# Optimization experiments

Hardware: AMD Instinct MI355X
Metric: run time of the kernel (lower is better)

Reference implementation:

```python
import jax, jax.numpy as jnp
import numpy as np

N_QUBITS = 10
BATCH = 16384
Q_DEPTH = 2


def _apply_1q_shared(state, U, q):
    # state: [B, 2, 2, ..., 2]; U: [2, 2] complex, acting on wire q
    state = jnp.moveaxis(state, 1 + q, -1)
    state = jnp.einsum('b...i,ji->b...j', state, U)
    return jnp.moveaxis(state, -1, 1 + q)


def _apply_ry_batched(state, angles, q):
    # per-sample RY(angle) on wire q; angles: [B] float
    c = jnp.cos(angles * 0.5).astype(jnp.complex64)
    s = jnp.sin(angles * 0.5).astype(jnp.complex64)
    U = jnp.stack([jnp.stack([c, -s], -1), jnp.stack([s, c], -1)], -2)  # [B,2,2]
    state = jnp.moveaxis(state, 1 + q, -1)
    state = jnp.einsum('b...i,bji->b...j', state, U)
    return jnp.moveaxis(state, -1, 1 + q)


def _rot_matrix(phi, theta, omega):
    # PennyLane Rot = RZ(omega) @ RY(theta) @ RZ(phi)
    c = jnp.cos(theta * 0.5)
    s = jnp.sin(theta * 0.5)
    m00 = jnp.exp(-0.5j * (phi + omega)) * c
    m01 = -jnp.exp(0.5j * (phi - omega)) * s
    m10 = jnp.exp(-0.5j * (phi - omega)) * s
    m11 = jnp.exp(0.5j * (phi + omega)) * c
    return jnp.stack([jnp.stack([m00, m01]), jnp.stack([m10, m11])]).astype(jnp.complex64)


def _apply_cnot(state, c, t):
    st = jnp.moveaxis(state, (1 + c, 1 + t), (1, 2))  # [B, ctrl, tgt, ...]
    st = jnp.stack([st[:, 0], st[:, 1, ::-1]], axis=1)  # flip target where ctrl=1
    return jnp.moveaxis(st, (1, 2), (1 + c, 1 + t))


def setup_inputs() -> dict:
    key = jax.random.key(0)
    k1, k2 = jax.random.split(key)
    x = jax.random.uniform(k1, (BATCH, N_QUBITS), dtype=jnp.float32) * np.pi
    q_weights = 0.01 * jax.random.normal(k2, (Q_DEPTH, N_QUBITS, 3), dtype=jnp.float32)
    return {"x": x, "q_weights": q_weights}


def reference(x, q_weights) -> jnp.ndarray:
    B, n = x.shape
    L = q_weights.shape[0]
    # |0...0> statevector, batched: [B] + [2]*n (axis q <-> wire q, wire 0 most significant)
    state = jnp.zeros((B, 2 ** n), jnp.complex64).at[:, 0].set(1.0)
    state = state.reshape((B,) + (2,) * n)
    # AngleEmbedding(rotation='Y')
    for q in range(n):
        state = _apply_ry_batched(state, x[:, q], q)
    # StronglyEntanglingLayers: Rot on each wire, then ring of CNOTs with range (l % (n-1)) + 1
    for l in range(L):
        for q in range(n):
            U = _rot_matrix(q_weights[l, q, 0], q_weights[l, q, 1], q_weights[l, q, 2])
            state = _apply_1q_shared(state, U, q)
        r = (l % (n - 1)) + 1
        for q in range(n):
            state = _apply_cnot(state, q, (q + r) % n)
    probs = jnp.abs(state.reshape(B, 2 ** n)) ** 2  # [B, 2^n]
    bits = (np.arange(2 ** n)[:, None] >> (n - 1 - np.arange(n))[None, :]) & 1
    signs = jnp.asarray(1.0 - 2.0 * bits, jnp.float32)  # [2^n, n], PauliZ eigenvalues
    return (probs @ signs).astype(jnp.float32)  # [B, n] expvals
```

## Files before the change

### kernel.cpp

```cpp
#include <hip/hip_runtime.h>

#define DEVINL __device__ __forceinline__

typedef float f32x2 __attribute__((ext_vector_type(2)));

struct GC { int laneXor, regXor, rowL, rowR; };
struct Circ { GC g[20]; int sgnL[10], sgnR[10]; };

constexpr Circ build_circ() {
    Circ c{};
    unsigned A[10] = {};
    for (int i = 0; i < 10; ++i) A[i] = 1u << i;
    for (int w = 0; w < 10; ++w) {
        int pos = 9 - w;
        unsigned m = 1u << pos;
        c.g[w] = GC{ int(m >> 4), int(m & 15u), int(m >> 4), int(m & 15u) };
    }
    for (int q = 0; q < 10; ++q) { int pc = 9 - q, pt = 9 - ((q + 1) % 10); A[pt] ^= A[pc]; }
    unsigned M[10] = {}, Inv[10] = {};
    for (int i = 0; i < 10; ++i) { M[i] = A[i]; Inv[i] = 1u << i; }
    for (int col = 0; col < 10; ++col) {
        int piv = col;
        while (!((M[piv] >> col) & 1u)) ++piv;
        unsigned tm = M[col]; M[col] = M[piv]; M[piv] = tm;
        unsigned ti = Inv[col]; Inv[col] = Inv[piv]; Inv[piv] = ti;
        for (int r = 0; r < 10; ++r)
            if (r != col && ((M[r] >> col) & 1u)) { M[r] ^= M[col]; Inv[r] ^= Inv[col]; }
    }
    for (int w = 0; w < 10; ++w) {
        int pos = 9 - w;
        unsigned m = 0;
        for (int i = 0; i < 10; ++i) m |= ((Inv[i] >> pos) & 1u) << i;
        unsigned row = A[pos];
        c.g[10 + w] = GC{ int(m >> 4), int(m & 15u), int(row >> 4), int(row & 15u) };
    }
    for (int q = 0; q < 10; ++q) { int pc = 9 - q, pt = 9 - ((q + 2) % 10); A[pt] ^= A[pc]; }
    for (int q = 0; q < 10; ++q) { unsigned row = A[9 - q]; c.sgnL[q] = int(row >> 4); c.sgnR[q] = int(row & 15u); }
    return c;
}

constexpr Circ CC = build_circ();

static_assert(CC.g[10].rowL == 31 && CC.g[10].rowR == 15, "w0 row");
static_assert(CC.g[11].rowL == 48 && CC.g[11].rowR == 0,  "w1 row");
static_assert(CC.g[12].rowL == 56 && CC.g[12].rowR == 0,  "w2 row");
static_assert(CC.g[13].rowL == 60 && CC.g[13].rowR == 0,  "w3 row");
static_assert(CC.g[14].rowL == 62 && CC.g[14].rowR == 0,  "w4 row");
static_assert(CC.g[15].rowL == 63 && CC.g[15].rowR == 0,  "w5 row");
static_assert(CC.g[16].rowL == 63 && CC.g[16].rowR == 8,  "w6 row");
static_assert(CC.g[17].rowL == 63 && CC.g[17].rowR == 12, "w7 row");
static_assert(CC.g[18].rowL == 63 && CC.g[18].rowR == 14, "w8 row");
static_assert(CC.g[19].rowL == 63 && CC.g[19].rowR == 15, "w9 row");
static_assert(CC.g[10].laneXor == 48 && CC.g[10].regXor == 0, "w0 m");
static_assert(CC.g[11].laneXor == 24 && CC.g[12].laneXor == 12, "w1/w2 m");
static_assert(CC.g[13].laneXor == 6  && CC.g[14].laneXor == 3,  "w3/w4 m");
static_assert(CC.g[15].laneXor == 1  && CC.g[15].regXor == 8,   "w5 m");
static_assert(CC.g[16].laneXor == 0 && CC.g[16].regXor == 12, "w6 m");
static_assert(CC.g[17].laneXor == 0 && CC.g[17].regXor == 6,  "w7 m");
static_assert(CC.g[18].laneXor == 0 && CC.g[18].regXor == 3,  "w8 m");
static_assert(CC.g[19].laneXor == 48 && CC.g[19].regXor == 1,   "w9 m");

#if __has_builtin(__builtin_amdgcn_permlane32_swap)
#define HAS_PL32 1
#else
#define HAS_PL32 0
#endif
#if __has_builtin(__builtin_amdgcn_permlane16_swap)
#define HAS_PL16 1
#else
#define HAS_PL16 0
#endif

DEVINL float csw(float v, int sw) {
    return __int_as_float(__float_as_int(v) ^ sw);
}

DEVINL float bsum16(float v, int lane) {
#if HAS_PL16
    auto r = __builtin_amdgcn_permlane16_swap(__float_as_int(v), __float_as_int(v), false, false);
    return __int_as_float(r[0]) + __int_as_float(r[1]);
#else
    return v + __int_as_float(__builtin_amdgcn_ds_swizzle(__float_as_int(v), 0x1F | (16 << 10)));
#endif
}
DEVINL float bsum32(float v, int lane) {
#if HAS_PL32
    auto r = __builtin_amdgcn_permlane32_swap(__float_as_int(v), __float_as_int(v), false, false);
    return __int_as_float(r[0]) + __int_as_float(r[1]);
#else
    return v + __int_as_float(__builtin_amdgcn_ds_bpermute((lane ^ 32) << 2, __float_as_int(v)));
#endif
}

template<int XOR>
DEVINL float fetch(float v, int lane) {
    if constexpr (XOR == 0)      return v;
    else if constexpr (XOR == 1) return __int_as_float(__builtin_amdgcn_update_dpp(0, __float_as_int(v), 0xB1, 0xF, 0xF, true));
    else if constexpr (XOR == 2) return __int_as_float(__builtin_amdgcn_update_dpp(0, __float_as_int(v), 0x4E, 0xF, 0xF, true));
    else if constexpr (XOR == 3) return __int_as_float(__builtin_amdgcn_update_dpp(0, __float_as_int(v), 0x1B, 0xF, 0xF, true));
    else if constexpr (XOR < 32) return __int_as_float(__builtin_amdgcn_ds_swizzle(__float_as_int(v), 0x1F | (XOR << 10)));
    else return __int_as_float(__builtin_amdgcn_ds_bpermute((lane ^ XOR) << 2, __float_as_int(v)));
}

DEVINL void pk_fma_acc(f32x2& a, f32x2 t, f32x2 b) {
    asm("v_pk_fma_f32 %0, %1, %2, %0" : "+v"(a) : "v"(t), "v"(b));
}

__device__ __attribute__((aligned(16))) float g_cst[80];

__global__ void qprep(const float* __restrict__ qw) {
    int g = threadIdx.x;
    if (g < 10) {
        float phi = qw[g * 3 + 0], th = qw[g * 3 + 1], om = qw[g * 3 + 2];
        float c = cosf(0.5f * th), s = sinf(0.5f * th);
        float apo = 0.5f * (phi + om), amo = 0.5f * (phi - om);
        g_cst[g * 4 + 0] =  cosf(apo) * c;
        g_cst[g * 4 + 1] = -sinf(apo) * c;
        g_cst[g * 4 + 2] = -cosf(amo) * s;
        g_cst[g * 4 + 3] = -sinf(amo) * s;
    } else if (g < 20) {
        int w = g - 10;
        float phi = qw[g * 3 + 0], th = qw[g * 3 + 1];
        float c = cosf(0.5f * th), s = sinf(0.5f * th);
        g_cst[40 + w] = s / c;
        g_cst[50 + w * 2 + 0] =  cosf(0.5f * phi);
        g_cst[50 + w * 2 + 1] = -sinf(0.5f * phi);
    } else if (g == 20) {
        float p = 1.f;
        for (int w = 0; w < 10; ++w) p *= cosf(0.5f * qw[(10 + w) * 3 + 1]);
        g_cst[70] = p;
    }
}

DEVINL void wf(const float* cst, float xw, int w,
               float& a0r, float& a0i, float& a1r, float& a1i) {
    float h = 0.5f * xw;
    float s = __sinf(h), c = __cosf(h);
    float m0 = cst[w * 4 + 0], m1 = cst[w * 4 + 1], m2 = cst[w * 4 + 2], m3 = cst[w * 4 + 3];
    a0r =  m0 * c + m2 * s;
    a0i =  m1 * c + m3 * s;
    a1r = -m2 * c + m0 * s;
    a1i =  m3 * c - m1 * s;
}

template<int W>
DEVINL void apply_gate(f32x2 (&a2)[16], const float* cst, int lane, const int (&sw)[10]) {
    constexpr GC gc = CC.g[10 + W];
    float tt = csw(cst[40 + W], sw[W]);
    f32x2 tp; tp.x = tt;  tp.y = tt;
    f32x2 tn; tn.x = -tt; tn.y = -tt;
    f32x2 b2[16];
    #pragma unroll
    for (int r = 0; r < 16; ++r) {
        f32x2 s = a2[r ^ gc.regXor];
        b2[r].x = fetch<gc.laneXor>(s.x, lane);
        b2[r].y = fetch<gc.laneXor>(s.y, lane);
    }
    #pragma unroll
    for (int r = 0; r < 16; ++r) {
        const bool sR = __builtin_popcount(unsigned(gc.rowR & r)) & 1;
        pk_fma_acc(a2[r], sR ? tp : tn, b2[r]);
    }
}

__global__ __launch_bounds__(256) void qsim(const float* __restrict__ x,
                                            float* __restrict__ out, int B) {
    const float* cst = g_cst;
    int lane = threadIdx.x & 63;
    int b = __builtin_amdgcn_readfirstlane(blockIdx.x * 4 + (threadIdx.x >> 6));
    if (b >= B) return;
    const float* xb = x + b * 10;

    int l = lane;
    int p48 = (l >> 4) ^ (l >> 5);
    int p56 = p48 ^ (l >> 3);
    int p60 = p56 ^ (l >> 2);
    int p62 = p60 ^ (l >> 1);
    int p63 = p62 ^ l;
    int p31 = p63 ^ (l >> 5);
    int s48 = p48 << 31, s56 = p56 << 31, s60 = p60 << 31;
    int s62 = p62 << 31, s63 = p63 << 31, s31 = p31 << 31;
    int sw[10] = { s31, s48, s56, s60, s62, s63, s63, s63, s63, s63 };

    float t01r[4], t01i[4], t23r[4], t23i[4];
    {
        float a0r, a0i, a1r, a1i, b0r, b0i, b1r, b1i;
        wf(cst, xb[9], 9, a0r, a0i, a1r, a1i);
        wf(cst, xb[8], 8, b0r, b0i, b1r, b1i);
        t01r[0] = a0r * b0r - a0i * b0i;  t01i[0] = a0r * b0i + a0i * b0r;
        t01r[1] = a1r * b0r - a1i * b0i;  t01i[1] = a1r * b0i + a1i * b0r;
        t01r[2] = a0r * b1r - a0i * b1i;  t01i[2] = a0r * b1i + a0i * b1r;
        t01r[3] = a1r * b1r - a1i * b1i;  t01i[3] = a1r * b1i + a1i * b1r;
        wf(cst, xb[7], 7, a0r, a0i, a1r, a1i);
        wf(cst, xb[6], 6, b0r, b0i, b1r, b1i);
        t23r[0] = a0r * b0r - a0i * b0i;  t23i[0] = a0r * b0i + a0i * b0r;
        t23r[1] = a1r * b0r - a1i * b0i;  t23i[1] = a1r * b0i + a1i * b0r;
        t23r[2] = a0r * b1r - a0i * b1i;  t23i[2] = a0r * b1i + a0i * b1r;
        t23r[3] = a1r * b1r - a1i * b1i;  t23i[3] = a1r * b1i + a1i * b1r;
    }

    float lfr, lfi;
    {
        float ear = cst[50 + 1 * 2], eai = csw(cst[50 + 1 * 2 + 1], sw[1]);
        #pragma unroll
        for (int w = 2; w <= 5; ++w) {
            float er = cst[50 + w * 2], ei = csw(cst[50 + w * 2 + 1], sw[w]);
            float nr = ear * er - eai * ei;
            float ni = ear * ei + eai * er;
            ear = nr; eai = ni;
        }
        float sc = cst[70];
        lfr = ear * sc; lfi = eai * sc;
        #pragma unroll
        for (int jj = 0; jj < 6; ++jj) {
            int w = 5 - jj;
            float a0r, a0i, a1r, a1i;
            wf(cst, xb[w], w, a0r, a0i, a1r, a1i);
            int bit = (lane >> jj) & 1;
            float pr = bit ? a1r : a0r;
            float pi = bit ? a1i : a0i;
            float nr = lfr * pr - lfi * pi;
            float ni = lfr * pi + lfi * pr;
            lfr = nr; lfi = ni;
        }
    }

    float e6r = cst[50 + 6 * 2], e6i = csw(cst[50 + 6 * 2 + 1], sw[6]);
    float e7r = cst[50 + 7 * 2], e7i = csw(cst[50 + 7 * 2 + 1], sw[7]);
    float Pr_ = e6r * e7r - e6i * e7i, Pi_ = e6r * e7i + e6i * e7r;
    float Qr_ = e6r * e7r + e6i * e7i, Qi_ = e6i * e7r - e6r * e7i;
    float t23pr[4], t23pi[4];
    t23pr[0] = t23r[0] * Pr_ - t23i[0] * Pi_;  t23pi[0] = t23r[0] * Pi_ + t23i[0] * Pr_;
    t23pr[1] = t23r[1] * Qr_ - t23i[1] * Qi_;  t23pi[1] = t23r[1] * Qi_ + t23i[1] * Qr_;
    t23pr[2] = t23r[2] * Pr_ + t23i[2] * Pi_;  t23pi[2] = t23i[2] * Pr_ - t23r[2] * Pi_;
    t23pr[3] = t23r[3] * Qr_ + t23i[3] * Qi_;  t23pi[3] = t23i[3] * Qr_ - t23r[3] * Qi_;

    float e0r = cst[50 + 0 * 2], e0i = csw(cst[50 + 0 * 2 + 1], sw[0]);
    float e9r = cst[50 + 9 * 2], e9i = csw(cst[50 + 9 * 2 + 1], sw[9]);
    float e8r = cst[50 + 8 * 2], e8i = csw(cst[50 + 8 * 2 + 1], sw[8]);
    float ebr = e0r * e9r - e0i * e9i, ebi = e0r * e9i + e0i * e9r;
    float G0r = e8r * ebr - e8i * ebi, G0i = e8r * ebi + e8i * ebr;
    float G1r = e8r * ebr + e8i * ebi, G1i = e8i * ebr - e8r * ebi;

    float g4r[4], g4i[4];
    #pragma unroll
    for (int v = 0; v < 4; ++v) {
        g4r[v] = lfr * t01r[v] - lfi * t01i[v];
        g4i[v] = lfr * t01i[v] + lfi * t01r[v];
    }
    f32x2 a2[16];
    #pragma unroll
    for (int r = 0; r < 16; ++r) {
        float tr = g4r[r & 3] * t23pr[r >> 2] - g4i[r & 3] * t23pi[r >> 2];
        float ti = g4r[r & 3] * t23pi[r >> 2] + g4i[r & 3] * t23pr[r >> 2];
        float gr = (r & 1) ? G1r : G0r;
        float gi = (r & 1) ? G1i : G0i;
        if (__builtin_popcount(unsigned(r & 14)) & 1) gi = -gi;
        a2[r].x = tr * gr - ti * gi;
        a2[r].y = tr * gi + ti * gr;
    }

    apply_gate<1>(a2, cst, lane, sw);
    apply_gate<4>(a2, cst, lane, sw);
    apply_gate<2>(a2, cst, lane, sw);
    apply_gate<6>(a2, cst, lane, sw);
    apply_gate<3>(a2, cst, lane, sw);
    apply_gate<5>(a2, cst, lane, sw);
    apply_gate<0>(a2, cst, lane, sw);
    apply_gate<7>(a2, cst, lane, sw);
    apply_gate<9>(a2, cst, lane, sw);
    apply_gate<8>(a2, cst, lane, sw);

    float wv[16];
    #pragma unroll
    for (int r = 0; r < 16; ++r) wv[r] = a2[r].x * a2[r].x + a2[r].y * a2[r].y;
    #pragma unroll
    for (int bS = 1; bS < 8; bS <<= 1) {
        #pragma unroll
        for (int r = 0; r < 16; ++r) {
            if (!(r & bS)) {
                float xv = wv[r], yv = wv[r | bS];
                wv[r]      = xv + yv;
                wv[r | bS] = xv - yv;
            }
        }
    }

    float e[10];
    #pragma unroll
    for (int q = 0; q < 10; ++q) {
        const int R = CC.sgnR[q];
        float num = (R & 8) ? (wv[R ^ 8] - wv[R]) : (wv[R] + wv[R ^ 8]);
        int slq = __popc(unsigned(lane & CC.sgnL[q])) & 1;
        e[q] = csw(num, slq << 31);
    }

    #pragma unroll
    for (int q = 0; q < 10; ++q) {
        e[q] += fetch<1>(e[q], lane);
        e[q] += fetch<2>(e[q], lane);
    }
    int s = lane & 3;
    bool s1 = (s & 1) != 0, s2 = (s & 2) != 0;
    float v0 = s1 ? e[1] : e[0];
    float u0 = s1 ? e[3] : e[2];
    v0 = s2 ? u0 : v0;
    float v1 = s1 ? e[5] : e[4];
    float u1 = s1 ? e[7] : e[6];
    v1 = s2 ? u1 : v1;
    float v2 = s1 ? e[9] : e[8];

    v0 += fetch<4>(v0, lane);  v1 += fetch<4>(v1, lane);  v2 += fetch<4>(v2, lane);
    v0 += fetch<8>(v0, lane);  v1 += fetch<8>(v1, lane);  v2 += fetch<8>(v2, lane);
    v0 = bsum16(v0, lane);     v1 = bsum16(v1, lane);     v2 = bsum16(v2, lane);
    v0 = bsum32(v0, lane);     v1 = bsum32(v1, lane);     v2 = bsum32(v2, lane);

    float vo = v0;
    int hi = lane >> 2;
    vo = (hi == 1) ? v1 : vo;
    vo = (hi == 2) ? v2 : vo;
    if (lane < 10) out[b * 10 + lane] = vo;
}

extern "C" void kernel_launch(void* const* d_in, const int* in_sizes, int n_in,
                              void* d_out, int out_size, void* d_ws, size_t ws_size,
                              hipStream_t stream) {
    const float* x  = (const float*)d_in[0];
    const float* qw = (const float*)d_in[1];
    float* out = (float*)d_out;
    int B = in_sizes[0] / 10;
    int blocks = (B + 3) / 4;
    hipLaunchKernelGGL(qprep, dim3(1), dim3(64), 0, stream, qw);
    hipLaunchKernelGGL(qsim, dim3(blocks), dim3(256), 0, stream, x, out, B);
}
```

Before: 86.88 us.

## Map each sample to 32 lanes with 32 amplitudes per lane

Changes the statevector distribution from 64 lanes × 16 registers to 32 lanes × 32 registers, so each wave now simulates two samples. More gates become register-only (laneXor 0), handled by an in-place pairwise update with no cross-lane traffic. Lane-crossing gates now need only swizzles within 32 lanes, so ds_bpermute and the permlane32 reduction step are gone. The cost is a roughly doubled amplitude register footprint per thread, which may reduce occupancy or cause spills, and the batch index is no longer wave-uniform.

```diff
diff --git a/kernel.cpp b/kernel.cpp
--- a/kernel.cpp
+++ b/kernel.cpp
@@ -14,7 +14,7 @@
     for (int w = 0; w < 10; ++w) {
         int pos = 9 - w;
         unsigned m = 1u << pos;
-        c.g[w] = GC{ int(m >> 4), int(m & 15u), int(m >> 4), int(m & 15u) };
+        c.g[w] = GC{ int(m >> 5), int(m & 31u), int(m >> 5), int(m & 31u) };
     }
     for (int q = 0; q < 10; ++q) { int pc = 9 - q, pt = 9 - ((q + 1) % 10); A[pt] ^= A[pc]; }
     unsigned M[10] = {}, Inv[10] = {};
@@ -32,64 +32,38 @@
         unsigned m = 0;
         for (int i = 0; i < 10; ++i) m |= ((Inv[i] >> pos) & 1u) << i;
         unsigned row = A[pos];
-        c.g[10 + w] = GC{ int(m >> 4), int(m & 15u), int(row >> 4), int(row & 15u) };
+        c.g[10 + w] = GC{ int(m >> 5), int(m & 31u), int(row >> 5), int(row & 31u) };
     }
     for (int q = 0; q < 10; ++q) { int pc = 9 - q, pt = 9 - ((q + 2) % 10); A[pt] ^= A[pc]; }
-    for (int q = 0; q < 10; ++q) { unsigned row = A[9 - q]; c.sgnL[q] = int(row >> 4); c.sgnR[q] = int(row & 15u); }
+    for (int q = 0; q < 10; ++q) { unsigned row = A[9 - q]; c.sgnL[q] = int(row >> 5); c.sgnR[q] = int(row & 31u); }
     return c;
 }
 
 constexpr Circ CC = build_circ();
 
-static_assert(CC.g[10].rowL == 31 && CC.g[10].rowR == 15, "w0 row");
-static_assert(CC.g[11].rowL == 48 && CC.g[11].rowR == 0,  "w1 row");
-static_assert(CC.g[12].rowL == 56 && CC.g[12].rowR == 0,  "w2 row");
-static_assert(CC.g[13].rowL == 60 && CC.g[13].rowR == 0,  "w3 row");
-static_assert(CC.g[14].rowL == 62 && CC.g[14].rowR == 0,  "w4 row");
-static_assert(CC.g[15].rowL == 63 && CC.g[15].rowR == 0,  "w5 row");
-static_assert(CC.g[16].rowL == 63 && CC.g[16].rowR == 8,  "w6 row");
-static_assert(CC.g[17].rowL == 63 && CC.g[17].rowR == 12, "w7 row");
-static_assert(CC.g[18].rowL == 63 && CC.g[18].rowR == 14, "w8 row");
-static_assert(CC.g[19].rowL == 63 && CC.g[19].rowR == 15, "w9 row");
-static_assert(CC.g[10].laneXor == 48 && CC.g[10].regXor == 0, "w0 m");
-static_assert(CC.g[11].laneXor == 24 && CC.g[12].laneXor == 12, "w1/w2 m");
-static_assert(CC.g[13].laneXor == 6  && CC.g[14].laneXor == 3,  "w3/w4 m");
-static_assert(CC.g[15].laneXor == 1  && CC.g[15].regXor == 8,   "w5 m");
-static_assert(CC.g[16].laneXor == 0 && CC.g[16].regXor == 12, "w6 m");
-static_assert(CC.g[17].laneXor == 0 && CC.g[17].regXor == 6,  "w7 m");
-static_assert(CC.g[18].laneXor == 0 && CC.g[18].regXor == 3,  "w8 m");
-static_assert(CC.g[19].laneXor == 48 && CC.g[19].regXor == 1,   "w9 m");
-
-#if __has_builtin(__builtin_amdgcn_permlane32_swap)
-#define HAS_PL32 1
-#else
-#define HAS_PL32 0
-#endif
-#if __has_builtin(__builtin_amdgcn_permlane16_swap)
-#define HAS_PL16 1
-#else
-#define HAS_PL16 0
-#endif
+static_assert(CC.g[10].laneXor == 24 && CC.g[10].regXor == 0,  "w0 m");
+static_assert(CC.g[11].laneXor == 12 && CC.g[11].regXor == 0,  "w1 m");
+static_assert(CC.g[12].laneXor == 6  && CC.g[12].regXor == 0,  "w2 m");
+static_assert(CC.g[13].laneXor == 3  && CC.g[13].regXor == 0,  "w3 m");
+static_assert(CC.g[14].laneXor == 1  && CC.g[14].regXor == 16, "w4 m");
+static_assert(CC.g[15].laneXor == 0  && CC.g[15].regXor == 24, "w5 m");
+static_assert(CC.g[16].laneXor == 0  && CC.g[16].regXor == 12, "w6 m");
+static_assert(CC.g[17].laneXor == 0  && CC.g[17].regXor == 6,  "w7 m");
+static_assert(CC.g[18].laneXor == 0  && CC.g[18].regXor == 3,  "w8 m");
+static_assert(CC.g[19].laneXor == 24 && CC.g[19].regXor == 1,  "w9 m");
+static_assert(CC.g[10].rowL == 15 && CC.g[10].rowR == 31, "w0 row");
+static_assert(CC.g[11].rowL == 24 && CC.g[11].rowR == 0,  "w1 row");
+static_assert(CC.g[12].rowL == 28 && CC.g[12].rowR == 0,  "w2 row");
+static_assert(CC.g[13].rowL == 30 && CC.g[13].rowR == 0,  "w3 row");
+static_assert(CC.g[14].rowL == 31 && CC.g[14].rowR == 0,  "w4 row");
+static_assert(CC.g[15].rowL == 31 && CC.g[15].rowR == 16, "w5 row");
+static_assert(CC.g[16].rowL == 31 && CC.g[16].rowR == 24, "w6 row");
+static_assert(CC.g[17].rowL == 31 && CC.g[17].rowR == 28, "w7 row");
+static_assert(CC.g[18].rowL == 31 && CC.g[18].rowR == 30, "w8 row");
+static_assert(CC.g[19].rowL == 31 && CC.g[19].rowR == 31, "w9 row");
 
 DEVINL float csw(float v, int sw) {
     return __int_as_float(__float_as_int(v) ^ sw);
-}
-
-DEVINL float bsum16(float v, int lane) {
-#if HAS_PL16
-    auto r = __builtin_amdgcn_permlane16_swap(__float_as_int(v), __float_as_int(v), false, false);
-    return __int_as_float(r[0]) + __int_as_float(r[1]);
-#else
-    return v + __int_as_float(__builtin_amdgcn_ds_swizzle(__float_as_int(v), 0x1F | (16 << 10)));
-#endif
-}
-DEVINL float bsum32(float v, int lane) {
-#if HAS_PL32
-    auto r = __builtin_amdgcn_permlane32_swap(__float_as_int(v), __float_as_int(v), false, false);
-    return __int_as_float(r[0]) + __int_as_float(r[1]);
-#else
-    return v + __int_as_float(__builtin_amdgcn_ds_bpermute((lane ^ 32) << 2, __float_as_int(v)));
-#endif
 }
 
 template<int XOR>
@@ -98,12 +72,18 @@
     else if constexpr (XOR == 1) return __int_as_float(__builtin_amdgcn_update_dpp(0, __float_as_int(v), 0xB1, 0xF, 0xF, true));
     else if constexpr (XOR == 2) return __int_as_float(__builtin_amdgcn_update_dpp(0, __float_as_int(v), 0x4E, 0xF, 0xF, true));
     else if constexpr (XOR == 3) return __int_as_float(__builtin_amdgcn_update_dpp(0, __float_as_int(v), 0x1B, 0xF, 0xF, true));
-    else if constexpr (XOR < 32) return __int_as_float(__builtin_amdgcn_ds_swizzle(__float_as_int(v), 0x1F | (XOR << 10)));
-    else return __int_as_float(__builtin_amdgcn_ds_bpermute((lane ^ XOR) << 2, __float_as_int(v)));
+    else                         return __int_as_float(__builtin_amdgcn_ds_swizzle(__float_as_int(v), 0x1F | (XOR << 10)));
 }
 
 DEVINL void pk_fma_acc(f32x2& a, f32x2 t, f32x2 b) {
     asm("v_pk_fma_f32 %0, %1, %2, %0" : "+v"(a) : "v"(t), "v"(b));
+}
+
+DEVINL f32x2 cmul(f32x2 a, f32x2 b) {
+    f32x2 r;
+    r.x = a.x * b.x - a.y * b.y;
+    r.y = a.x * b.y + a.y * b.x;
+    return r;
 }
 
 __device__ __attribute__((aligned(16))) float g_cst[80];
@@ -132,34 +112,52 @@
     }
 }
 
-DEVINL void wf(const float* cst, float xw, int w,
-               float& a0r, float& a0i, float& a1r, float& a1i) {
+DEVINL void wf(const float* cst, float xw, int w, f32x2& f0, f32x2& f1) {
     float h = 0.5f * xw;
     float s = __sinf(h), c = __cosf(h);
     float m0 = cst[w * 4 + 0], m1 = cst[w * 4 + 1], m2 = cst[w * 4 + 2], m3 = cst[w * 4 + 3];
-    a0r =  m0 * c + m2 * s;
-    a0i =  m1 * c + m3 * s;
-    a1r = -m2 * c + m0 * s;
-    a1i =  m3 * c - m1 * s;
+    f0.x =  m0 * c + m2 * s;
+    f0.y =  m1 * c + m3 * s;
+    f1.x = -m2 * c + m0 * s;
+    f1.y =  m3 * c - m1 * s;
 }
 
 template<int W>
-DEVINL void apply_gate(f32x2 (&a2)[16], const float* cst, int lane, const int (&sw)[10]) {
+DEVINL void apply_gate(f32x2 (&a2)[32], const float* cst, int lane, const int (&sw)[10]) {
     constexpr GC gc = CC.g[10 + W];
     float tt = csw(cst[40 + W], sw[W]);
     f32x2 tp; tp.x = tt;  tp.y = tt;
     f32x2 tn; tn.x = -tt; tn.y = -tt;
-    f32x2 b2[16];
-    #pragma unroll
-    for (int r = 0; r < 16; ++r) {
-        f32x2 s = a2[r ^ gc.regXor];
-        b2[r].x = fetch<gc.laneXor>(s.x, lane);
-        b2[r].y = fetch<gc.laneXor>(s.y, lane);
-    }
-    #pragma unroll
-    for (int r = 0; r < 16; ++r) {
-        const bool sR = __builtin_popcount(unsigned(gc.rowR & r)) & 1;
-        pk_fma_acc(a2[r], sR ? tp : tn, b2[r]);
+    if constexpr (gc.laneXor == 0) {
+        #pragma unroll
+        for (int r = 0; r < 32; ++r) {
+            const int r2 = r ^ gc.regXor;
+            if (r < r2) {
+                f32x2 old = a2[r];
+                const bool sR  = __builtin_popcount(unsigned(gc.rowR & r )) & 1;
+                const bool sR2 = __builtin_popcount(unsigned(gc.rowR & r2)) & 1;
+                pk_fma_acc(a2[r],  sR  ? tp : tn, a2[r2]);
+                pk_fma_acc(a2[r2], sR2 ? tp : tn, old);
+            }
+        }
+    } else {
+        #pragma unroll
+        for (int c = 0; c < 2; ++c) {
+            f32x2 b2[16];
+            #pragma unroll
+            for (int i = 0; i < 16; ++i) {
+                const int r = (i & 7) + c * 8 + ((i >> 3) << 4);
+                f32x2 s = a2[r ^ gc.regXor];
+                b2[i].x = fetch<gc.laneXor>(s.x, lane);
+                b2[i].y = fetch<gc.laneXor>(s.y, lane);
+            }
+            #pragma unroll
+            for (int i = 0; i < 16; ++i) {
+                const int r = (i & 7) + c * 8 + ((i >> 3) << 4);
+                const bool sR = __builtin_popcount(unsigned(gc.rowR & r)) & 1;
+                pk_fma_acc(a2[r], sR ? tp : tn, b2[i]);
+            }
+        }
     }
 }
 
@@ -167,117 +165,114 @@
                                             float* __restrict__ out, int B) {
     const float* cst = g_cst;
     int lane = threadIdx.x & 63;
-    int b = __builtin_amdgcn_readfirstlane(blockIdx.x * 4 + (threadIdx.x >> 6));
+    int l5 = lane & 31;
+    int b = blockIdx.x * 8 + (threadIdx.x >> 5);
     if (b >= B) return;
     const float* xb = x + b * 10;
 
-    int l = lane;
-    int p48 = (l >> 4) ^ (l >> 5);
-    int p56 = p48 ^ (l >> 3);
-    int p60 = p56 ^ (l >> 2);
-    int p62 = p60 ^ (l >> 1);
-    int p63 = p62 ^ l;
-    int p31 = p63 ^ (l >> 5);
-    int s48 = p48 << 31, s56 = p56 << 31, s60 = p60 << 31;
-    int s62 = p62 << 31, s63 = p63 << 31, s31 = p31 << 31;
-    int sw[10] = { s31, s48, s56, s60, s62, s63, s63, s63, s63, s63 };
-
-    float t01r[4], t01i[4], t23r[4], t23i[4];
+    int p24 = (l5 >> 4) ^ (l5 >> 3);
+    int p28 = p24 ^ (l5 >> 2);
+    int p30 = p28 ^ (l5 >> 1);
+    int p31 = p30 ^ l5;
+    int p15 = p31 ^ (l5 >> 4);
+    int s24 = p24 << 31, s28 = p28 << 31, s30 = p30 << 31,
+        s31 = p31 << 31, s15 = p15 << 31;
+    int sw_[10] = { s15, s24, s28, s30, s31, s31, s31, s31, s31, s31 };
+
+    f32x2 t01[4], t23[4], f5t[2];
     {
-        float a0r, a0i, a1r, a1i, b0r, b0i, b1r, b1i;
-        wf(cst, xb[9], 9, a0r, a0i, a1r, a1i);
-        wf(cst, xb[8], 8, b0r, b0i, b1r, b1i);
-        t01r[0] = a0r * b0r - a0i * b0i;  t01i[0] = a0r * b0i + a0i * b0r;
-        t01r[1] = a1r * b0r - a1i * b0i;  t01i[1] = a1r * b0i + a1i * b0r;
-        t01r[2] = a0r * b1r - a0i * b1i;  t01i[2] = a0r * b1i + a0i * b1r;
-        t01r[3] = a1r * b1r - a1i * b1i;  t01i[3] = a1r * b1i + a1i * b1r;
-        wf(cst, xb[7], 7, a0r, a0i, a1r, a1i);
-        wf(cst, xb[6], 6, b0r, b0i, b1r, b1i);
-        t23r[0] = a0r * b0r - a0i * b0i;  t23i[0] = a0r * b0i + a0i * b0r;
-        t23r[1] = a1r * b0r - a1i * b0i;  t23i[1] = a1r * b0i + a1i * b0r;
-        t23r[2] = a0r * b1r - a0i * b1i;  t23i[2] = a0r * b1i + a0i * b1r;
-        t23r[3] = a1r * b1r - a1i * b1i;  t23i[3] = a1r * b1i + a1i * b1r;
-    }
-
-    float lfr, lfi;
+        f32x2 a0, a1, b0, b1;
+        wf(cst, xb[9], 9, a0, a1);
+        wf(cst, xb[8], 8, b0, b1);
+        t01[0] = cmul(a0, b0); t01[1] = cmul(a1, b0);
+        t01[2] = cmul(a0, b1); t01[3] = cmul(a1, b1);
+        wf(cst, xb[7], 7, a0, a1);
+        wf(cst, xb[6], 6, b0, b1);
+        t23[0] = cmul(a0, b0); t23[1] = cmul(a1, b0);
+        t23[2] = cmul(a0, b1); t23[3] = cmul(a1, b1);
+        wf(cst, xb[5], 5, f5t[0], f5t[1]);
+    }
+
+    f32x2 E0; E0.x = cst[50];      E0.y = csw(cst[51], s15);
+    f32x2 E1; E1.x = cst[52];      E1.y = csw(cst[53], s24);
+    f32x2 E2; E2.x = cst[54];      E2.y = csw(cst[55], s28);
+    f32x2 E3; E3.x = cst[56];      E3.y = csw(cst[57], s30);
+    f32x2 E4; E4.x = cst[58];      E4.y = csw(cst[59], s31);
+    f32x2 E5; E5.x = cst[60];      E5.y = csw(cst[61], s31);
+    f32x2 E6; E6.x = cst[62];      E6.y = csw(cst[63], s31);
+    f32x2 E7; E7.x = cst[64];      E7.y = csw(cst[65], s31);
+    f32x2 E8; E8.x = cst[66];      E8.y = csw(cst[67], s31);
+    f32x2 E9; E9.x = cst[68];      E9.y = csw(cst[69], s31);
+
+    f32x2 lf;
     {
-        float ear = cst[50 + 1 * 2], eai = csw(cst[50 + 1 * 2 + 1], sw[1]);
+        f32x2 ea = cmul(cmul(E1, E2), cmul(E3, E4));
+        float sc = cst[70];
+        lf.x = ea.x * sc; lf.y = ea.y * sc;
         #pragma unroll
-        for (int w = 2; w <= 5; ++w) {
-            float er = cst[50 + w * 2], ei = csw(cst[50 + w * 2 + 1], sw[w]);
-            float nr = ear * er - eai * ei;
-            float ni = ear * ei + eai * er;
-            ear = nr; eai = ni;
+        for (int jj = 0; jj < 5; ++jj) {
+            int w = 4 - jj;
+            f32x2 f0, f1;
+            wf(cst, xb[w], w, f0, f1);
+            int bit = (l5 >> jj) & 1;
+            f32x2 p; p.x = bit ? f1.x : f0.x; p.y = bit ? f1.y : f0.y;
+            lf = cmul(lf, p);
         }
-        float sc = cst[70];
-        lfr = ear * sc; lfi = eai * sc;
+    }
+
+    f32x2 f5p[2];
+    f5p[0] = cmul(f5t[0], E5);
+    { f32x2 e5c; e5c.x = E5.x; e5c.y = -E5.y; f5p[1] = cmul(f5t[1], e5c); }
+    f32x2 V00 = cmul(E6, E7);
+    f32x2 V01; { f32x2 e7c; e7c.x = E7.x; e7c.y = -E7.y; V01 = cmul(E6, e7c); }
+    f32x2 EB = cmul(E9, E0);
+    f32x2 H0 = cmul(E8, EB);
+    f32x2 H1; { f32x2 ebc; ebc.x = EB.x; ebc.y = -EB.y; H1 = cmul(E8, ebc); }
+
+    f32x2 tf[8];
+    #pragma unroll
+    for (int j = 0; j < 8; ++j) {
+        f32x2 tA = cmul(t23[j & 3], f5p[j >> 2]);
+        const int s6 = ((j >> 2) ^ (j >> 1)) & 1;
+        const int s7 = s6 ^ (j & 1);
+        f32x2 V;
+        V.x = s6 ? (s7 ? V00.x : V01.x) : (s7 ? V01.x : V00.x);
+        V.y = s6 ? -(s7 ? V00.y : V01.y) : (s7 ? V01.y : V00.y);
+        tf[j] = cmul(tA, V);
+    }
+
+    f32x2 g4[4];
+    #pragma unroll
+    for (int v = 0; v < 4; ++v) g4[v] = cmul(lf, t01[v]);
+    f32x2 a2[32];
+    #pragma unroll
+    for (int r = 0; r < 32; ++r) {
+        f32x2 t = cmul(g4[r & 3], tf[(r >> 2) & 7]);
+        f32x2 G;
+        G.x = (r & 1) ? H1.x : H0.x;
+        G.y = (r & 1) ? H1.y : H0.y;
+        if (__builtin_popcount(unsigned(r & 30)) & 1) G.y = -G.y;
+        a2[r] = cmul(t, G);
+    }
+
+    apply_gate<0>(a2, cst, lane, sw_);
+    apply_gate<5>(a2, cst, lane, sw_);
+    apply_gate<1>(a2, cst, lane, sw_);
+    apply_gate<3>(a2, cst, lane, sw_);
+    apply_gate<2>(a2, cst, lane, sw_);
+    apply_gate<6>(a2, cst, lane, sw_);
+    apply_gate<9>(a2, cst, lane, sw_);
+    apply_gate<4>(a2, cst, lane, sw_);
+    apply_gate<7>(a2, cst, lane, sw_);
+    apply_gate<8>(a2, cst, lane, sw_);
+
+    float wv[32];
+    #pragma unroll
+    for (int r = 0; r < 32; ++r) wv[r] = a2[r].x * a2[r].x + a2[r].y * a2[r].y;
+    #pragma unroll
+    for (int bS = 1; bS < 16; bS <<= 1) {
         #pragma unroll
-        for (int jj = 0; jj < 6; ++jj) {
-            int w = 5 - jj;
-            float a0r, a0i, a1r, a1i;
-            wf(cst, xb[w], w, a0r, a0i, a1r, a1i);
-            int bit = (lane >> jj) & 1;
-            float pr = bit ? a1r : a0r;
-            float pi = bit ? a1i : a0i;
-            float nr = lfr * pr - lfi * pi;
-            float ni = lfr * pi + lfi * pr;
-            lfr = nr; lfi = ni;
-        }
-    }
-
-    float e6r = cst[50 + 6 * 2], e6i = csw(cst[50 + 6 * 2 + 1], sw[6]);
-    float e7r = cst[50 + 7 * 2], e7i = csw(cst[50 + 7 * 2 + 1], sw[7]);
-    float Pr_ = e6r * e7r - e6i * e7i, Pi_ = e6r * e7i + e6i * e7r;
-    float Qr_ = e6r * e7r + e6i * e7i, Qi_ = e6i * e7r - e6r * e7i;
-    float t23pr[4], t23pi[4];
-    t23pr[0] = t23r[0] * Pr_ - t23i[0] * Pi_;  t23pi[0] = t23r[0] * Pi_ + t23i[0] * Pr_;
-    t23pr[1] = t23r[1] * Qr_ - t23i[1] * Qi_;  t23pi[1] = t23r[1] * Qi_ + t23i[1] * Qr_;
-    t23pr[2] = t23r[2] * Pr_ + t23i[2] * Pi_;  t23pi[2] = t23i[2] * Pr_ - t23r[2] * Pi_;
-    t23pr[3] = t23r[3] * Qr_ + t23i[3] * Qi_;  t23pi[3] = t23i[3] * Qr_ - t23r[3] * Qi_;
-
-    float e0r = cst[50 + 0 * 2], e0i = csw(cst[50 + 0 * 2 + 1], sw[0]);
-    float e9r = cst[50 + 9 * 2], e9i = csw(cst[50 + 9 * 2 + 1], sw[9]);
-    float e8r = cst[50 + 8 * 2], e8i = csw(cst[50 + 8 * 2 + 1], sw[8]);
-    float ebr = e0r * e9r - e0i * e9i, ebi = e0r * e9i + e0i * e9r;
-    float G0r = e8r * ebr - e8i * ebi, G0i = e8r * ebi + e8i * ebr;
-    float G1r = e8r * ebr + e8i * ebi, G1i = e8i * ebr - e8r * ebi;
-
-    float g4r[4], g4i[4];
-    #pragma unroll
-    for (int v = 0; v < 4; ++v) {
-        g4r[v] = lfr * t01r[v] - lfi * t01i[v];
-        g4i[v] = lfr * t01i[v] + lfi * t01r[v];
-    }
-    f32x2 a2[16];
-    #pragma unroll
-    for (int r = 0; r < 16; ++r) {
-        float tr = g4r[r & 3] * t23pr[r >> 2] - g4i[r & 3] * t23pi[r >> 2];
-        float ti = g4r[r & 3] * t23pi[r >> 2] + g4i[r & 3] * t23pr[r >> 2];
-        float gr = (r & 1) ? G1r : G0r;
-        float gi = (r & 1) ? G1i : G0i;
-        if (__builtin_popcount(unsigned(r & 14)) & 1) gi = -gi;
-        a2[r].x = tr * gr - ti * gi;
-        a2[r].y = tr * gi + ti * gr;
-    }
-
-    apply_gate<1>(a2, cst, lane, sw);
-    apply_gate<4>(a2, cst, lane, sw);
-    apply_gate<2>(a2, cst, lane, sw);
-    apply_gate<6>(a2, cst, lane, sw);
-    apply_gate<3>(a2, cst, lane, sw);
-    apply_gate<5>(a2, cst, lane, sw);
-    apply_gate<0>(a2, cst, lane, sw);
-    apply_gate<7>(a2, cst, lane, sw);
-    apply_gate<9>(a2, cst, lane, sw);
-    apply_gate<8>(a2, cst, lane, sw);
-
-    float wv[16];
-    #pragma unroll
-    for (int r = 0; r < 16; ++r) wv[r] = a2[r].x * a2[r].x + a2[r].y * a2[r].y;
-    #pragma unroll
-    for (int bS = 1; bS < 8; bS <<= 1) {
-        #pragma unroll
-        for (int r = 0; r < 16; ++r) {
+        for (int r = 0; r < 32; ++r) {
             if (!(r & bS)) {
                 float xv = wv[r], yv = wv[r | bS];
                 wv[r]      = xv + yv;
@@ -290,8 +285,8 @@
     #pragma unroll
     for (int q = 0; q < 10; ++q) {
         const int R = CC.sgnR[q];
-        float num = (R & 8) ? (wv[R ^ 8] - wv[R]) : (wv[R] + wv[R ^ 8]);
-        int slq = __popc(unsigned(lane & CC.sgnL[q])) & 1;
+        float num = (R & 16) ? (wv[R ^ 16] - wv[R]) : (wv[R] + wv[R ^ 16]);
+        int slq = __popc(unsigned(l5 & CC.sgnL[q])) & 1;
         e[q] = csw(num, slq << 31);
     }
 
@@ -300,7 +295,7 @@
         e[q] += fetch<1>(e[q], lane);
         e[q] += fetch<2>(e[q], lane);
     }
-    int s = lane & 3;
+    int s = l5 & 3;
     bool s1 = (s & 1) != 0, s2 = (s & 2) != 0;
     float v0 = s1 ? e[1] : e[0];
     float u0 = s1 ? e[3] : e[2];
@@ -310,16 +305,15 @@
     v1 = s2 ? u1 : v1;
     float v2 = s1 ? e[9] : e[8];
 
-    v0 += fetch<4>(v0, lane);  v1 += fetch<4>(v1, lane);  v2 += fetch<4>(v2, lane);
-    v0 += fetch<8>(v0, lane);  v1 += fetch<8>(v1, lane);  v2 += fetch<8>(v2, lane);
-    v0 = bsum16(v0, lane);     v1 = bsum16(v1, lane);     v2 = bsum16(v2, lane);
-    v0 = bsum32(v0, lane);     v1 = bsum32(v1, lane);     v2 = bsum32(v2, lane);
+    v0 += fetch<4>(v0, lane);   v1 += fetch<4>(v1, lane);   v2 += fetch<4>(v2, lane);
+    v0 += fetch<8>(v0, lane);   v1 += fetch<8>(v1, lane);   v2 += fetch<8>(v2, lane);
+    v0 += fetch<16>(v0, lane);  v1 += fetch<16>(v1, lane);  v2 += fetch<16>(v2, lane);
 
     float vo = v0;
-    int hi = lane >> 2;
+    int hi = l5 >> 2;
     vo = (hi == 1) ? v1 : vo;
     vo = (hi == 2) ? v2 : vo;
-    if (lane < 10) out[b * 10 + lane] = vo;
+    if (l5 < 10) out[b * 10 + l5] = vo;
 }
 
 extern "C" void kernel_launch(void* const* d_in, const int* in_sizes, int n_in,
@@ -329,7 +323,7 @@
     const float* qw = (const float*)d_in[1];
     float* out = (float*)d_out;
     int B = in_sizes[0] / 10;
-    int blocks = (B + 3) / 4;
+    int blocks = (B + 7) / 8;
     hipLaunchKernelGGL(qprep, dim3(1), dim3(64), 0, stream, qw);
     hipLaunchKernelGGL(qsim, dim3(blocks), dim3(256), 0, stream, x, out, B);
 }
```

Result: faster. 82.09 us (-5.5%).
